# Performance work log

Hardware: AMD Instinct MI355X
Metric: run time of the kernel (lower is better)

The kernel has to match this reference:

```python
import jax, jax.numpy as jnp
import numpy as np

NEG = 9999.0
EPS = 1e-8  # torch CosineSimilarity default eps


def _attend_head(x, v, W_out, b_out):
    # x: [B, n, D]; row 0 is the node, rows 1: are neighbours
    node = x[:, 0, :]            # [B, D]
    neigh = x[:, 1:, :]          # [B, n-1, D]
    scores = jnp.einsum('bnd,bd->bn', neigh, node)  # [B, n-1]
    # masked_softmax: positions with exactly-zero score get -9999 added
    masked = scores + (jnp.where(scores != 0, 0.0, -1.0) * NEG)
    aw = jax.nn.softmax(masked, axis=-1)            # [B, n-1]
    context = jnp.einsum('n,bn,bnd->bd', v, aw, neigh)  # [B, D]
    feat = jnp.concatenate([node, context], axis=1)     # [B, 2D]
    return feat @ W_out.T + b_out                       # [B, 300]


def _cosine(a, b):
    na = jnp.maximum(jnp.linalg.norm(a, axis=1), EPS)
    nb = jnp.maximum(jnp.linalg.norm(b, axis=1), EPS)
    return jnp.sum(a * b, axis=1) / (na * nb)


def setup_inputs() -> dict:
    key = jax.random.key(0)
    ks = jax.random.split(key, 8)
    B, n, V, D = 4096, 32, 100000, 512
    inputs = jax.random.randint(ks[0], (B, 2, n), 0, V, dtype=jnp.int64)
    inputs_prop = jax.random.randint(ks[1], (B, 2, 3, n), 0, V, dtype=jnp.int64)
    emb = jax.random.normal(ks[2], (V, D), dtype=jnp.float32)
    W_out = jax.random.normal(ks[3], (300, 2 * D), dtype=jnp.float32) * 0.02
    b_out = jax.random.normal(ks[4], (300,), dtype=jnp.float32) * 0.02
    v = jnp.full((n - 1,), 1.0 / (n - 1), dtype=jnp.float32)
    W_prop = jax.random.normal(ks[5], (300, 600 + D), dtype=jnp.float32) * 0.02
    b_prop = jax.random.normal(ks[6], (300,), dtype=jnp.float32) * 0.02
    return {"inputs": inputs, "inputs_prop": inputs_prop, "emb": emb,
            "W_out": W_out, "b_out": b_out, "v": v,
            "W_prop": W_prop, "b_prop": b_prop}


def reference(inputs, inputs_prop, emb, W_out, b_out, v, W_prop, b_prop):
    # entity branch
    results = []
    for i in range(2):
        x = emb[inputs[:, i, :]]                 # [B, n, D]
        results.append(_attend_head(x, v, W_out, b_out))
    # property branch
    prop_vecs = []
    for i in range(2):
        xp = emb[inputs_prop[:, i]]              # [B, 3, n, D]
        dom = _attend_head(xp[:, 1], v, W_out, b_out)   # domain
        rng = _attend_head(xp[:, 2], v, W_out, b_out)   # range
        prp = xp[:, 0, 0, :]                     # property embedding [B, D]
        feat = jnp.concatenate([dom, rng, prp], axis=1)  # [B, 1112]
        prop_vecs.append(feat @ W_prop.T + b_prop)
    x_ent = _cosine(results[0], results[1])
    x_prop = _cosine(prop_vecs[0], prop_vecs[1])
    return jnp.concatenate([x_ent, x_prop])
```

## Files before the change

### kernel.cpp

```cpp
#include <hip/hip_runtime.h>

typedef _Float16 f16x8 __attribute__((ext_vector_type(8)));
typedef _Float16 f16x4 __attribute__((ext_vector_type(4)));
typedef _Float16 f16x2 __attribute__((ext_vector_type(2)));
typedef float    f32x4 __attribute__((ext_vector_type(4)));
typedef float    f32x4v __attribute__((ext_vector_type(4)));

#define EMBH_OFF  0ULL
#define CTXH_OFF  102400000ULL
#define APH_OFF   127565824ULL
#define WH_OFF    138051584ULL
#define WPH_OFF   138706944ULL
#define HEAD_OFF  139444224ULL
#define PROP_OFF  149274624ULL
#define NIDX_OFF  159105024ULL
#define PIDX_OFF  159203328ULL

__device__ __forceinline__ void gload16h(const _Float16* g, _Float16* l) {
    __builtin_amdgcn_global_load_lds(
        (const __attribute__((address_space(1))) unsigned int*)g,
        (__attribute__((address_space(3))) unsigned int*)l, 16, 0, 0);
}

__global__ __launch_bounds__(256) void conv_kernel(
    const float* __restrict__ emb, const float* __restrict__ W_out,
    const float* __restrict__ W_prop,
    _Float16* __restrict__ embh, _Float16* __restrict__ Wh, _Float16* __restrict__ Wph)
{
    if (blockIdx.x < 128) {
        const int N_WH4  = 81920;
        const int N_WPH4 = 92160;
        int stride = 128 * 256;
        for (int id = blockIdx.x * 256 + threadIdx.x; id < N_WH4 + N_WPH4; id += stride) {
            f32x4 f; _Float16* dst;
            if (id < N_WH4) {
                int n = id >> 8, c4 = id & 255;
                f = (n < 300) ? __builtin_nontemporal_load(((const f32x4v*)W_out) + n * 256 + c4)
                              : (f32x4){0.f,0.f,0.f,0.f};
                dst = Wh + (size_t)id * 4;
            } else {
                int id3 = id - N_WH4;
                int n = id3 / 288, c4 = id3 - n * 288;
                if (n >= 300 || (c4 >= 150 && c4 < 160)) f = (f32x4){0.f,0.f,0.f,0.f};
                else if (c4 < 150) f = __builtin_nontemporal_load(((const f32x4v*)W_prop) + n * 278 + c4);
                else               f = __builtin_nontemporal_load(((const f32x4v*)W_prop) + n * 278 + c4 - 10);
                dst = Wph + (size_t)id3 * 4;
            }
            f16x4 h = { (_Float16)f.x, (_Float16)f.y, (_Float16)f.z, (_Float16)f.w };
            *(f16x4*)dst = h;
        }
    } else {
        const int NU_EMB = 6400000;
        int nb = gridDim.x - 128;
        int stride = nb * 256;
        const f32x4v* src = (const f32x4v*)emb;
        f16x8* dst = (f16x8*)embh;
        for (int u = (blockIdx.x - 128) * 256 + threadIdx.x; u < NU_EMB; u += stride) {
            f32x4 a = __builtin_nontemporal_load(src + 2 * u);
            f32x4 b = __builtin_nontemporal_load(src + 2 * u + 1);
            f16x8 h = { (_Float16)a.x, (_Float16)a.y, (_Float16)a.z, (_Float16)a.w,
                        (_Float16)b.x, (_Float16)b.y, (_Float16)b.z, (_Float16)b.w };
            dst[u] = h;
        }
    }
}

__global__ __launch_bounds__(256) void attend_kernel(
    const int* __restrict__ inputs,
    const int* __restrict__ inputs_prop,
    const _Float16* __restrict__ embh,
    const float* __restrict__ v,
    _Float16* __restrict__ ctxh,
    int* __restrict__ nidx, int* __restrict__ pidx,
    _Float16* __restrict__ Aph)
{
    int w    = blockIdx.x * 4 + (threadIdx.x >> 6);
    int lane = threadIdx.x & 63;
    int h = w >> 12;
    int b = w & 4095;

    int base, i = 0;
    const int* ip;
    if (h < 2) { base = (b * 2 + h) * 32; ip = inputs; }
    else {
        i = (h - 2) >> 1;
        int s = 1 + ((h - 2) & 1);
        base = ((b * 2 + i) * 3 + s) * 32;
        ip = inputs_prop;
    }

    int myidx = 0;
    if (lane < 32) myidx = ip[base + lane];
    int idx0 = __shfl(myidx, 0);
    if (lane == 0) {
        nidx[w] = idx0;
        if (h == 2 || h == 4) pidx[i * 4096 + b] = inputs_prop[((b * 2 + i) * 3) * 32];
    }

    const f16x8* e8 = (const f16x8*)embh;
    f16x8 n8 = e8[(size_t)idx0 * 64 + lane];

    f16x8 pe[4];
    #pragma unroll
    for (int j = 1; j <= 4; ++j) {
        int ij = __shfl(myidx, j);
        pe[(j - 1) & 3] = e8[(size_t)ij * 64 + lane];
    }

    float m = -3.0e38f, den = 0.0f;
    float c[8] = {0.f,0.f,0.f,0.f,0.f,0.f,0.f,0.f};

    #pragma unroll
    for (int j = 1; j < 32; ++j) {
        const int slot = (j - 1) & 3;
        f16x8 ev = pe[slot];
        if (j + 4 < 32) {
            int ijn = __shfl(myidx, j + 4);
            pe[slot] = e8[(size_t)ijn * 64 + lane];
        }
        float p = 0.0f;
        const f16x2* na = (const f16x2*)&n8;
        const f16x2* ea = (const f16x2*)&ev;
#if __has_builtin(__builtin_amdgcn_fdot2)
        #pragma unroll
        for (int q = 0; q < 4; ++q) p = __builtin_amdgcn_fdot2(ea[q], na[q], p, false);
#else
        #pragma unroll
        for (int q = 0; q < 8; ++q) p += (float)ev[q] * (float)n8[q];
#endif
        #pragma unroll
        for (int d = 1; d < 64; d <<= 1) p += __shfl_xor(p, d);

        float s = (p != 0.0f) ? p : -9999.0f;
        if (s - m > 8.0f) {
            float scale = __expf(m - s);
            den *= scale;
            #pragma unroll
            for (int q = 0; q < 8; ++q) c[q] *= scale;
            m = s;
        }
        float e = __expf(s - m);
        den += e;
        float we = v[j - 1] * e;
        #pragma unroll
        for (int q = 0; q < 8; ++q) c[q] += we * (float)ev[q];
    }
    float inv = 1.0f / den;
    f16x8 co;
    #pragma unroll
    for (int q = 0; q < 8; ++q) co[q] = (_Float16)(c[q] * inv);
    *(f16x8*)(ctxh + (size_t)w * 512 + lane * 8) = co;

    if ((h == 2 || h == 4) && lane < 5) {
        f16x8 z = {};
        *(f16x8*)(Aph + (size_t)(i * 4096 + b) * 640 + 600 + lane * 8) = z;
    }
}

__global__ __launch_bounds__(192) void gemm_head_kernel(
    const _Float16* __restrict__ embh, const _Float16* __restrict__ ctxh,
    const int* __restrict__ nidx, const _Float16* __restrict__ Wh,
    const float* __restrict__ bias, float* __restrict__ outf,
    _Float16* __restrict__ Aph)
{
    __shared__ _Float16 Ash[48 * 64];
    __shared__ _Float16 Bsh[320 * 64];
    __shared__ int sN[48];

    int t = threadIdx.x, lane = t & 63, wid = t >> 6;
    int m0 = blockIdx.x * 48;
    if (t < 48) sN[t] = nidx[m0 + t];
    __syncthreads();

    f32x4 acc[20];
    #pragma unroll
    for (int nf = 0; nf < 20; ++nf) acc[nf] = (f32x4){0.f,0.f,0.f,0.f};

    int rowq = lane >> 3, cq = lane & 7;
    int cqs = cq ^ rowq;
    int l15 = lane & 15, hi = lane >> 4, l7 = lane & 7;

    for (int k0 = 0; k0 < 1024; k0 += 64) {
        #pragma unroll
        for (int qq = 0; qq < 16; ++qq) {
            int q = wid * 16 + qq;
            if (q < 6) {
                int row = q * 8 + rowq;
                if (k0 < 512) gload16h(embh + (size_t)sN[row] * 512 + k0 + cqs * 8, Ash + q * 512);
                else          gload16h(ctxh + (size_t)(m0 + row) * 512 + (k0 - 512) + cqs * 8, Ash + q * 512);
            } else if (q < 46) {
                int j = q - 6;
                int row = j * 8 + rowq;
                gload16h(Wh + (size_t)row * 1024 + k0 + cqs * 8, Bsh + j * 512);
            }
        }
        __syncthreads();

        #pragma unroll
        for (int s = 0; s < 2; ++s) {
            int sw = ((s * 4 + hi) ^ l7) * 8;
            f16x8 a = *(const f16x8*)&Ash[(wid * 16 + l15) * 64 + sw];
            #pragma unroll
            for (int nf = 0; nf < 20; ++nf) {
                f16x8 bb = *(const f16x8*)&Bsh[(nf * 16 + l15) * 64 + sw];
                acc[nf] = __builtin_amdgcn_mfma_f32_16x16x32_f16(a, bb, acc[nf], 0, 0, 0);
            }
        }
        __syncthreads();
    }

    #pragma unroll
    for (int nf = 0; nf < 20; ++nf) {
        int n = nf * 16 + l15;
        if (n >= 300) continue;
        int rowbase = m0 + wid * 16 + (hi << 2);
        float bv = bias[n];
        #pragma unroll
        for (int r = 0; r < 4; ++r) {
            float val = acc[nf][r] + bv;
            int mm = rowbase + r;
            int h = mm >> 12;
            if (h < 2) {
                outf[(size_t)mm * 300 + n] = val;
            } else {
                int i = (h - 2) >> 1;
                int col = ((h - 2) & 1) ? 300 + n : n;
                Aph[(size_t)(i * 4096 + (mm & 4095)) * 640 + col] = (_Float16)val;
            }
        }
    }
}

__global__ __launch_bounds__(256) void gemm_prop_kernel(
    const _Float16* __restrict__ Aph, const int* __restrict__ pidx,
    const _Float16* __restrict__ embh, const _Float16* __restrict__ Wph,
    const float* __restrict__ bias, float* __restrict__ outf)
{
    __shared__ _Float16 Ash[32 * 64];
    __shared__ _Float16 Bsh[320 * 64];
    __shared__ int sPid[32];

    int t = threadIdx.x, lane = t & 63, wid = t >> 6;
    int wm = wid >> 1, wn = wid & 1;
    int m0 = blockIdx.x * 32;
    if (t < 32) {
        int mm = m0 + t;
        sPid[t] = pidx[(mm >> 12) * 4096 + (mm & 4095)];
    }
    __syncthreads();

    f32x4 acc[10];
    #pragma unroll
    for (int nf = 0; nf < 10; ++nf) acc[nf] = (f32x4){0.f,0.f,0.f,0.f};

    int rowq = lane >> 3, cq = lane & 7;
    int cqs = cq ^ rowq;
    int l15 = lane & 15, hi = lane >> 4, l7 = lane & 7;

    for (int k0 = 0; k0 < 1152; k0 += 64) {
        #pragma unroll
        for (int qq = 0; qq < 11; ++qq) {
            int q = wid * 11 + qq;
            if (q < 4) {
                int row = q * 8 + rowq;
                if (k0 < 640) gload16h(Aph + (size_t)(m0 + row) * 640 + k0 + cqs * 8, Ash + q * 512);
                else          gload16h(embh + (size_t)sPid[row] * 512 + (k0 - 640) + cqs * 8, Ash + q * 512);
            } else if (q < 44) {
                int j = q - 4;
                int row = j * 8 + rowq;
                gload16h(Wph + (size_t)row * 1152 + k0 + cqs * 8, Bsh + j * 512);
            }
        }
        __syncthreads();

        #pragma unroll
        for (int s = 0; s < 2; ++s) {
            int sw = ((s * 4 + hi) ^ l7) * 8;
            f16x8 a = *(const f16x8*)&Ash[(wm * 16 + l15) * 64 + sw];
            #pragma unroll
            for (int nf = 0; nf < 10; ++nf) {
                f16x8 bb = *(const f16x8*)&Bsh[((wn * 10 + nf) * 16 + l15) * 64 + sw];
                acc[nf] = __builtin_amdgcn_mfma_f32_16x16x32_f16(a, bb, acc[nf], 0, 0, 0);
            }
        }
        __syncthreads();
    }

    #pragma unroll
    for (int nf = 0; nf < 10; ++nf) {
        int n = wn * 160 + nf * 16 + l15;
        if (n >= 300) continue;
        int rowbase = m0 + wm * 16 + (hi << 2);
        float bv = bias[n];
        #pragma unroll
        for (int r = 0; r < 4; ++r)
            outf[(size_t)(rowbase + r) * 300 + n] = acc[nf][r] + bv;
    }
}

__global__ __launch_bounds__(256) void cosine_kernel(
    const float* __restrict__ head_out,
    const float* __restrict__ prop_out,
    float* __restrict__ out)
{
    int w    = blockIdx.x * 4 + (threadIdx.x >> 6);
    int lane = threadIdx.x & 63;
    const float *a, *b;
    if (w < 4096) {
        a = head_out + (size_t)w * 300;
        b = head_out + (size_t)(4096 + w) * 300;
    } else {
        int b2 = w - 4096;
        a = prop_out + (size_t)b2 * 300;
        b = prop_out + (size_t)(4096 + b2) * 300;
    }
    float ab = 0.f, aa = 0.f, bb = 0.f;
    for (int tt = lane; tt < 300; tt += 64) {
        float av = a[tt], bv = b[tt];
        ab += av * bv; aa += av * av; bb += bv * bv;
    }
    #pragma unroll
    for (int d = 1; d < 64; d <<= 1) {
        ab += __shfl_xor(ab, d);
        aa += __shfl_xor(aa, d);
        bb += __shfl_xor(bb, d);
    }
    if (lane == 0) {
        float na = fmaxf(sqrtf(aa), 1e-8f);
        float nb = fmaxf(sqrtf(bb), 1e-8f);
        out[w] = ab / (na * nb);
    }
}

extern "C" void kernel_launch(void* const* d_in, const int* in_sizes, int n_in,
                              void* d_out, int out_size, void* d_ws, size_t ws_size,
                              hipStream_t stream) {
    const int*   inputs      = (const int*)d_in[0];
    const int*   inputs_prop = (const int*)d_in[1];
    const float* emb         = (const float*)d_in[2];
    const float* W_out       = (const float*)d_in[3];
    const float* b_out       = (const float*)d_in[4];
    const float* v           = (const float*)d_in[5];
    const float* W_prop      = (const float*)d_in[6];
    const float* b_prop      = (const float*)d_in[7];
    float* out = (float*)d_out;

    char* ws = (char*)d_ws;
    _Float16* embh = (_Float16*)(ws + EMBH_OFF);
    _Float16* ctxh = (_Float16*)(ws + CTXH_OFF);
    _Float16* Aph  = (_Float16*)(ws + APH_OFF);
    _Float16* Wh   = (_Float16*)(ws + WH_OFF);
    _Float16* Wph  = (_Float16*)(ws + WPH_OFF);
    float* head_out = (float*)(ws + HEAD_OFF);
    float* prop_out = (float*)(ws + PROP_OFF);
    int*   nidx     = (int*)(ws + NIDX_OFF);
    int*   pidx     = (int*)(ws + PIDX_OFF);

    conv_kernel<<<8192, 256, 0, stream>>>(emb, W_out, W_prop, embh, Wh, Wph);
    attend_kernel<<<6144, 256, 0, stream>>>(inputs, inputs_prop, embh, v, ctxh, nidx, pidx, Aph);
    gemm_head_kernel<<<512, 192, 0, stream>>>(embh, ctxh, nidx, Wh, b_out, head_out, Aph);
    gemm_prop_kernel<<<256, 256, 0, stream>>>(Aph, pidx, embh, Wph, b_prop, prop_out);
    cosine_kernel<<<2048, 256, 0, stream>>>(head_out, prop_out, out);
}
```

Measured before the change: 241.1 us.

## Fuse property cosine into prop GEMM epilogue and use nontemporal emb stores

The prop GEMM now remaps its 32-row tile so it holds 16 batch rows from side 0 and the matching 16 rows from side 1. The epilogue stages the results in shared memory and computes the property cosine directly, so prop_out is no longer written to global memory or read back by a separate pass. The standalone cosine kernel shrinks to the entity half only. The fp16 embedding conversion also switches to nontemporal stores, which may hurt if embh reuse in L2 mattered for the following attend kernel.

```diff
diff --git a/kernel.cpp b/kernel.cpp
--- a/kernel.cpp
+++ b/kernel.cpp
@@ -60,7 +60,7 @@
             f32x4 b = __builtin_nontemporal_load(src + 2 * u + 1);
             f16x8 h = { (_Float16)a.x, (_Float16)a.y, (_Float16)a.z, (_Float16)a.w,
                         (_Float16)b.x, (_Float16)b.y, (_Float16)b.z, (_Float16)b.w };
-            dst[u] = h;
+            __builtin_nontemporal_store(h, dst + u);
         }
     }
 }
@@ -234,7 +234,7 @@
 __global__ __launch_bounds__(256) void gemm_prop_kernel(
     const _Float16* __restrict__ Aph, const int* __restrict__ pidx,
     const _Float16* __restrict__ embh, const _Float16* __restrict__ Wph,
-    const float* __restrict__ bias, float* __restrict__ outf)
+    const float* __restrict__ bias, float* __restrict__ out)
 {
     __shared__ _Float16 Ash[32 * 64];
     __shared__ _Float16 Bsh[320 * 64];
@@ -242,9 +242,9 @@
 
     int t = threadIdx.x, lane = t & 63, wid = t >> 6;
     int wm = wid >> 1, wn = wid & 1;
-    int m0 = blockIdx.x * 32;
+    int b0 = blockIdx.x * 16;
     if (t < 32) {
-        int mm = m0 + t;
+        int mm = ((t >> 4) << 12) + b0 + (t & 15);
         sPid[t] = pidx[(mm >> 12) * 4096 + (mm & 4095)];
     }
     __syncthreads();
@@ -263,7 +263,8 @@
             int q = wid * 11 + qq;
             if (q < 4) {
                 int row = q * 8 + rowq;
-                if (k0 < 640) gload16h(Aph + (size_t)(m0 + row) * 640 + k0 + cqs * 8, Ash + q * 512);
+                int mm = ((row >> 4) << 12) + b0 + (row & 15);
+                if (k0 < 640) gload16h(Aph + (size_t)mm * 640 + k0 + cqs * 8, Ash + q * 512);
                 else          gload16h(embh + (size_t)sPid[row] * 512 + (k0 - 640) + cqs * 8, Ash + q * 512);
             } else if (q < 44) {
                 int j = q - 4;
@@ -286,34 +287,51 @@
         __syncthreads();
     }
 
+    float* psm = (float*)Bsh;
     #pragma unroll
     for (int nf = 0; nf < 10; ++nf) {
         int n = wn * 160 + nf * 16 + l15;
         if (n >= 300) continue;
-        int rowbase = m0 + wm * 16 + (hi << 2);
+        int rowloc = wm * 16 + (hi << 2);
         float bv = bias[n];
         #pragma unroll
         for (int r = 0; r < 4; ++r)
-            outf[(size_t)(rowbase + r) * 300 + n] = acc[nf][r] + bv;
+            psm[(rowloc + r) * 304 + n] = acc[nf][r] + bv;
+    }
+    __syncthreads();
+
+    #pragma unroll
+    for (int bi = 0; bi < 4; ++bi) {
+        int bl = wid * 4 + bi;
+        const float* a = psm + bl * 304;
+        const float* bvv = psm + (16 + bl) * 304;
+        float ab = 0.f, aa = 0.f, bb = 0.f;
+        for (int tt = lane; tt < 300; tt += 64) {
+            float av = a[tt], bv2 = bvv[tt];
+            ab += av * bv2; aa += av * av; bb += bv2 * bv2;
+        }
+        #pragma unroll
+        for (int d = 1; d < 64; d <<= 1) {
+            ab += __shfl_xor(ab, d);
+            aa += __shfl_xor(aa, d);
+            bb += __shfl_xor(bb, d);
+        }
+        if (lane == 0) {
+            float na = fmaxf(sqrtf(aa), 1e-8f);
+            float nb = fmaxf(sqrtf(bb), 1e-8f);
+            out[4096 + b0 + bl] = ab / (na * nb);
+        }
     }
 }
 
 __global__ __launch_bounds__(256) void cosine_kernel(
     const float* __restrict__ head_out,
-    const float* __restrict__ prop_out,
     float* __restrict__ out)
 {
     int w    = blockIdx.x * 4 + (threadIdx.x >> 6);
     int lane = threadIdx.x & 63;
-    const float *a, *b;
-    if (w < 4096) {
-        a = head_out + (size_t)w * 300;
-        b = head_out + (size_t)(4096 + w) * 300;
-    } else {
-        int b2 = w - 4096;
-        a = prop_out + (size_t)b2 * 300;
-        b = prop_out + (size_t)(4096 + b2) * 300;
-    }
+    const float* a = head_out + (size_t)w * 300;
+    const float* b = head_out + (size_t)(4096 + w) * 300;
     float ab = 0.f, aa = 0.f, bb = 0.f;
     for (int tt = lane; tt < 300; tt += 64) {
         float av = a[tt], bv = b[tt];
@@ -352,13 +370,12 @@
     _Float16* Wh   = (_Float16*)(ws + WH_OFF);
     _Float16* Wph  = (_Float16*)(ws + WPH_OFF);
     float* head_out = (float*)(ws + HEAD_OFF);
-    float* prop_out = (float*)(ws + PROP_OFF);
     int*   nidx     = (int*)(ws + NIDX_OFF);
     int*   pidx     = (int*)(ws + PIDX_OFF);
 
     conv_kernel<<<8192, 256, 0, stream>>>(emb, W_out, W_prop, embh, Wh, Wph);
     attend_kernel<<<6144, 256, 0, stream>>>(inputs, inputs_prop, embh, v, ctxh, nidx, pidx, Aph);
     gemm_head_kernel<<<512, 192, 0, stream>>>(embh, ctxh, nidx, Wh, b_out, head_out, Aph);
-    gemm_prop_kernel<<<256, 256, 0, stream>>>(Aph, pidx, embh, Wph, b_prop, prop_out);
-    cosine_kernel<<<2048, 256, 0, stream>>>(head_out, prop_out, out);
-}
+    gemm_prop_kernel<<<256, 256, 0, stream>>>(Aph, pidx, embh, Wph, b_prop, out);
+    cosine_kernel<<<1024, 256, 0, stream>>>(head_out, out);
+}
```

Result: no change. 243.0 us (+0.8%).
